# Performance work log

Measured on AMD Instinct MI355X. Metric: run time of the kernel, lower is better.

The kernel has to match this reference:

```python
import jax, jax.numpy as jnp
import numpy as np

N = 50000
E = 800000
NODE_IN = 128
HID = 256
OUT = 256
EDGE_DIM = 16
HEADS = 4
CH = HID // HEADS  # 64
NEG_SLOPE = 0.2


def _init_linear(key, fan_in, fan_out):
    k1, k2 = jax.random.split(key)
    bound = 1.0 / np.sqrt(fan_in)
    W = jax.random.uniform(k1, (fan_in, fan_out), jnp.float32, -bound, bound)
    b = jax.random.uniform(k2, (fan_out,), jnp.float32, -bound, bound)
    return W, b


def setup_inputs() -> dict:
    key = jax.random.key(0)
    ks = jax.random.split(key, 12)
    node_feats = jax.random.normal(ks[0], (N, NODE_IN), jnp.float32)
    edge_index = jax.random.randint(ks[1], (2, E), 0, N, jnp.int64)
    edge_attr = jax.random.normal(ks[2], (E, EDGE_DIM), jnp.float32)

    Wnp, bnp = _init_linear(ks[3], NODE_IN, HID)           # node_proj
    Wep, bep = _init_linear(ks[4], EDGE_DIM, HID)          # edge_proj
    # GATConv 1: in = 2*HID, out per head = CH
    Wg1, _ = _init_linear(ks[5], 2 * HID, HEADS * CH)
    as1 = jax.random.normal(ks[6], (HEADS, CH), jnp.float32) * 0.1
    ad1 = jax.random.normal(ks[7], (HEADS, CH), jnp.float32) * 0.1
    bg1 = jnp.zeros((HEADS * CH,), jnp.float32)
    # GATConv 2: in = HID, out per head = OUT//HEADS
    Wg2, _ = _init_linear(ks[8], HID, HEADS * (OUT // HEADS))
    as2 = jax.random.normal(ks[9], (HEADS, OUT // HEADS), jnp.float32) * 0.1
    ad2 = jax.random.normal(ks[10], (HEADS, OUT // HEADS), jnp.float32) * 0.1
    bg2 = jnp.zeros((OUT,), jnp.float32)
    Wo, bo = _init_linear(ks[11], OUT, OUT)                # out_proj
    return {
        "node_feats": node_feats, "edge_attr": edge_attr,
        "Wnp": Wnp, "bnp": bnp, "Wep": Wep, "bep": bep,
        "Wg1": Wg1, "as1": as1, "ad1": ad1, "bg1": bg1,
        "Wg2": Wg2, "as2": as2, "ad2": ad2, "bg2": bg2,
        "Wo": Wo, "bo": bo,
        "edge_index": edge_index,
    }


def scatter_mean(src, index, num_nodes):
    # mean of edge features grouped by target node; empty groups -> 0 (count clamped to 1)
    s = jax.ops.segment_sum(src, index, num_segments=num_nodes)
    cnt = jax.ops.segment_sum(jnp.ones((src.shape[0],), src.dtype), index, num_segments=num_nodes)
    return s / jnp.maximum(cnt, 1.0)[:, None]


def gat_conv(x, src, dst, W, att_src, att_dst, bias, num_nodes, heads, ch):
    # PyG GATConv with add_self_loops=True (loops appended by caller via src/dst),
    # concat=True, negative_slope=0.2.
    xh = (x @ W).reshape(num_nodes, heads, ch)             # [N,H,C]
    a_src = jnp.sum(xh * att_src, axis=-1)                 # [N,H]
    a_dst = jnp.sum(xh * att_dst, axis=-1)                 # [N,H]
    logits = jax.nn.leaky_relu(a_src[src] + a_dst[dst], NEG_SLOPE)  # [E,H]
    # segment softmax over incoming edges of each destination node
    m = jax.ops.segment_max(logits, dst, num_segments=num_nodes)    # [N,H]
    ex = jnp.exp(logits - m[dst])
    denom = jax.ops.segment_sum(ex, dst, num_segments=num_nodes)    # [N,H]
    alpha = ex / denom[dst]                                          # [E,H]
    msg = xh[src] * alpha[:, :, None]                                # [E,H,C]
    out = jax.ops.segment_sum(msg, dst, num_segments=num_nodes)      # [N,H,C]
    return out.reshape(num_nodes, heads * ch) + bias


def reference(node_feats, edge_attr, Wnp, bnp, Wep, bep,
              Wg1, as1, ad1, bg1, Wg2, as2, ad2, bg2, Wo, bo, edge_index):
    n = node_feats.shape[0]
    x = node_feats @ Wnp + bnp                                       # [N,HID]
    # EdgeAggregator: mean of edge_attr over target nodes, then edge_proj
    nef = scatter_mean(edge_attr, edge_index[1], n)                  # [N,EDGE_DIM]
    nef = nef @ Wep + bep                                            # [N,HID]
    x = jnp.concatenate([x, nef], axis=-1)                           # [N,2*HID]
    # add self loops once (same augmented edge set for both GAT layers)
    loops = jnp.arange(n, dtype=edge_index.dtype)
    src = jnp.concatenate([edge_index[0], loops])
    dst = jnp.concatenate([edge_index[1], loops])
    x = jax.nn.elu(gat_conv(x, src, dst, Wg1, as1, ad1, bg1, n, HEADS, CH))
    # dropout is identity in eval mode
    x = jax.nn.elu(gat_conv(x, src, dst, Wg2, as2, ad2, bg2, n, HEADS, OUT // HEADS))
    return x @ Wo + bo
```

## Files before the change

### kernel.cpp

```cpp
#include <hip/hip_runtime.h>
#include <hip/hip_bf16.h>


#define HEADS 4

typedef __attribute__((ext_vector_type(8))) _Float16 f16x8;
typedef __attribute__((ext_vector_type(4))) float f32x4;
typedef __attribute__((ext_vector_type(4))) unsigned short u16x4;
typedef __attribute__((ext_vector_type(8))) unsigned short u16x8;

__device__ __forceinline__ unsigned short f2h(float v) {
    _Float16 h = (_Float16)v;
    return __builtin_bit_cast(unsigned short, h);
}
__device__ __forceinline__ float h2f(unsigned short u) {
    return (float)__builtin_bit_cast(_Float16, u);
}
__device__ __forceinline__ void split_hilo16(float v, unsigned short& h, unsigned short& l) {
    h = f2h(v);
    l = f2h(v - h2f(h));
}
__device__ __forceinline__ void gl2lds16(const unsigned short* g, unsigned short* l) {
    __builtin_amdgcn_global_load_lds(
        (const __attribute__((address_space(1))) unsigned int*)g,
        (__attribute__((address_space(3))) unsigned int*)l,
        16, 0, 0);
}


__global__ __launch_bounds__(256) void count_kernel(
    const int* __restrict__ dst, int* __restrict__ cnt, int E)
{
    int e = blockIdx.x * 256 + threadIdx.x;
    if (e < E) atomicAdd(&cnt[dst[e]], 1);
}

__global__ __launch_bounds__(256) void scan1_kernel(
    const int* __restrict__ cnt, int* __restrict__ chunk_sum, int N)
{
    __shared__ int sd[256];
    int t = threadIdx.x;
    int n = blockIdx.x * 256 + t;
    sd[t] = (n < N) ? (cnt[n] + 1) : 0;
    __syncthreads();
    for (int o = 128; o > 0; o >>= 1) {
        if (t < o) sd[t] += sd[t + o];
        __syncthreads();
    }
    if (t == 0) chunk_sum[blockIdx.x] = sd[0];
}

__global__ __launch_bounds__(256) void scan2_kernel(
    const int* __restrict__ chunk_sum, int* __restrict__ chunk_off, int nchunk)
{
    __shared__ int sd[256];
    __shared__ int carry;
    int t = threadIdx.x;
    if (t == 0) carry = 0;
    __syncthreads();
    for (int b = 0; b < nchunk; b += 256) {
        int i = b + t;
        int v = (i < nchunk) ? chunk_sum[i] : 0;
        sd[t] = v;
        __syncthreads();
        for (int o = 1; o < 256; o <<= 1) {
            int x = (t >= o) ? sd[t - o] : 0;
            __syncthreads();
            sd[t] += x;
            __syncthreads();
        }
        if (i < nchunk) chunk_off[i] = carry + sd[t] - v;
        __syncthreads();
        if (t == 0) carry += sd[255];
        __syncthreads();
    }
}

__global__ __launch_bounds__(256) void scan3_kernel(
    const int* __restrict__ cnt, const int* __restrict__ chunk_off,
    int* __restrict__ rowptr, int* __restrict__ fillptr,
    int* __restrict__ col, int* __restrict__ eid, int N)
{
    __shared__ int sd[256];
    int t = threadIdx.x;
    int n = blockIdx.x * 256 + t;
    int v = (n < N) ? (cnt[n] + 1) : 0;
    sd[t] = v;
    __syncthreads();
    for (int o = 1; o < 256; o <<= 1) {
        int x = (t >= o) ? sd[t - o] : 0;
        __syncthreads();
        sd[t] += x;
        __syncthreads();
    }
    if (n < N) {
        int incl = sd[t];
        int r = chunk_off[blockIdx.x] + incl - v;
        rowptr[n] = r;
        col[r] = n;
        eid[r] = -1;
        fillptr[n] = r + 1;
        if (n == N - 1) rowptr[N] = chunk_off[blockIdx.x] + incl;
    }
}

__global__ __launch_bounds__(256) void fill_kernel(
    const int* __restrict__ src, const int* __restrict__ dst,
    int* __restrict__ fillptr, int* __restrict__ col, int* __restrict__ eid, int E)
{
    int e = blockIdx.x * 256 + threadIdx.x;
    if (e >= E) return;
    int d = dst[e];
    int p = atomicAdd(&fillptr[d], 1);
    col[p] = src[e];
    eid[p] = e;
}

__global__ __launch_bounds__(256) void nef_csr_kernel(
    const float* __restrict__ ea, const int* __restrict__ rowptr,
    const int* __restrict__ eid,
    unsigned short* __restrict__ nefF, int N)
{
    int n = blockIdx.x * 4 + (threadIdx.x >> 6);
    if (n >= N) return;
    int t = threadIdx.x & 63;
    int f = t & 15, g = t >> 4;
    int base = rowptr[n], end = rowptr[n + 1];
    int deg = end - base - 1;
    float acc = 0.0f;
    for (int j = base + 1 + g; j < end; j += 4) {
        int e = eid[j];
        acc += ea[(size_t)e * 16 + f];
    }
    acc += __shfl_down(acc, 32, 64);
    acc += __shfl_down(acc, 16, 64);
    if (t < 16) {
        float v = acc / fmaxf((float)deg, 1.0f);
        nefF[(size_t)n * 32 + t] = f2h(v);
    } else if (t < 32) {
        nefF[(size_t)n * 32 + t] = 0;
    }
}

__global__ __launch_bounds__(256) void compose_w1_kernel(
    const float* __restrict__ Wnp, const float* __restrict__ Wep,
    const float* __restrict__ bnp, const float* __restrict__ bep,
    const float* __restrict__ Wg1,
    float* __restrict__ Wc, float* __restrict__ c1)
{
    int idx = blockIdx.x * 256 + threadIdx.x;
    if (idx >= 145 * 256) return;
    int i = idx >> 8, j = idx & 255;
    float s = 0.0f;
    if (i < 128) {
        for (int k = 0; k < 256; k++) s += Wnp[i * 256 + k] * Wg1[(size_t)k * 256 + j];
        Wc[i * 256 + j] = s;
    } else if (i < 144) {
        int ii = i - 128;
        for (int k = 0; k < 256; k++) s += Wep[ii * 256 + k] * Wg1[(size_t)(256 + k) * 256 + j];
        Wc[i * 256 + j] = s;
    } else {
        for (int k = 0; k < 256; k++)
            s += bnp[k] * Wg1[(size_t)k * 256 + j] + bep[k] * Wg1[(size_t)(256 + k) * 256 + j];
        c1[j] = s;
    }
}

__device__ __forceinline__ void pack_one(
    const float* __restrict__ W, int K, int KP, int idx,
    unsigned short* __restrict__ Ph, unsigned short* __restrict__ Pl)
{
    int tile = idx >> 9, w = idx & 511, lane = w >> 3, j = w & 7;
    int nk = KP >> 5;
    int ctile = tile / nk, t = tile % nk;
    int k = t * 32 + ((lane >> 4) << 3) + j;
    int n = (ctile << 4) + (lane & 15);
    float v = (k < K) ? W[(size_t)k * 256 + n] : 0.0f;
    unsigned short h, l;
    split_hilo16(v, h, l);
    Ph[idx] = h;
    Pl[idx] = l;
}

__global__ __launch_bounds__(256) void pack3_w_kernel(
    const float* __restrict__ Wc,  unsigned short* __restrict__ PcH,  unsigned short* __restrict__ PcL,
    const float* __restrict__ Wg2, unsigned short* __restrict__ Pg2H, unsigned short* __restrict__ Pg2L,
    const float* __restrict__ Wo,  unsigned short* __restrict__ PoH,  unsigned short* __restrict__ PoL)
{
    const int S0 = 160 * 256;
    const int S1 = S0 + 256 * 256;
    const int S2 = S1 + 256 * 256;
    int idx = blockIdx.x * 256 + threadIdx.x;
    if (idx < S0) {
        pack_one(Wc, 144, 160, idx, PcH, PcL);
    } else if (idx < S1) {
        pack_one(Wg2, 256, 256, idx - S0, Pg2H, Pg2L);
    } else if (idx < S2) {
        pack_one(Wo, 256, 256, idx - S1, PoH, PoL);
    }
}

template <int KSTEPS, int AMODE, int OMODE, bool FUSE_ATT>
__global__ __launch_bounds__(256, 4) void mfma_gemm_kernel(
    const unsigned short* __restrict__ Ah, const unsigned short* __restrict__ Al,
    const float* __restrict__ Af32,
    int lda,
    const unsigned short* __restrict__ Ph, const unsigned short* __restrict__ Pl,
    const float* __restrict__ bias,
    float* __restrict__ Cf,
    unsigned short* __restrict__ Ch, unsigned short* __restrict__ Cl,
    int ldc, int col_off, int Nrows,
    const float* __restrict__ att_src, const float* __restrict__ att_dst,
    float* __restrict__ a_srcO, float* __restrict__ a_dstO)
{
    __shared__ unsigned short ldsB[2][2][8][512];
    int tid = threadIdx.x;
    int wave = tid >> 6, lane = tid & 63;
    int quad = lane >> 4, m16 = lane & 15;
    int rowblk = blockIdx.x, colhalf = blockIdx.y;
    int ctile0 = colhalf * 8;

    int row = rowblk * 64 + wave * 16 + m16;
    bool rowok = row < Nrows;

    auto stage = [&](int t, int buf) {
        #pragma unroll
        for (int q = 0; q < 2; q++) {
            int c = wave * 2 + q;
            size_t gb = ((size_t)((ctile0 + c) * KSTEPS + t)) * 512 + lane * 8;
            gl2lds16(Ph + gb, &ldsB[buf][0][c][0]);
            gl2lds16(Pl + gb, &ldsB[buf][1][c][0]);
        }
    };

    u16x8 aH[KSTEPS];
    u16x8 aL[AMODE == 0 ? KSTEPS : 1];
    f32x4 aF[AMODE == 3 ? 2 * KSTEPS : 1];
    #pragma unroll
    for (int t = 0; t < KSTEPS; t++) {
        if (AMODE == 3) {
            if (t < KSTEPS - 1) {
                aF[2 * t] = (f32x4){};
                aF[2 * t + 1] = (f32x4){};
                if (rowok) {
                    const float* p = Af32 + (size_t)row * 128 + t * 32 + quad * 8;
                    aF[2 * t]     = *(const f32x4*)p;
                    aF[2 * t + 1] = *(const f32x4*)(p + 4);
                }
            } else {
                aH[t] = (u16x8){};
                if (rowok) aH[t] = *(const u16x8*)(Ah + (size_t)row * 32 + quad * 8);
            }
        } else {
            int k = t * 32 + quad * 8;
            aH[t] = (u16x8){};
            if (rowok) aH[t] = *(const u16x8*)(Ah + (size_t)row * lda + k);
            if (AMODE == 0) {
                aL[t] = (u16x8){};
                if (rowok) aL[t] = *(const u16x8*)(Al + (size_t)row * lda + k);
            }
        }
    }

    f32x4 acc[8] = {};
    stage(0, 0);
    __syncthreads();

    #pragma unroll
    for (int t = 0; t < KSTEPS; t++) {
        const int buf = t & 1;
        if (t + 1 < KSTEPS) stage(t + 1, buf ^ 1);

        f16x8 a_h, a_l;
        if (AMODE == 3 && t < KSTEPS - 1) {
            #pragma unroll
            for (int i = 0; i < 4; i++) {
                ((_Float16*)&a_h)[i]     = (_Float16)aF[2 * t][i];
                ((_Float16*)&a_h)[4 + i] = (_Float16)aF[2 * t + 1][i];
            }
        } else {
            a_h = __builtin_bit_cast(f16x8, aH[t]);
        }
        if (AMODE == 0) a_l = __builtin_bit_cast(f16x8, aL[t]);

        #pragma unroll
        for (int c = 0; c < 8; c++) {
            f16x8 b_h = __builtin_bit_cast(f16x8, *(const u16x8*)&ldsB[buf][0][c][lane * 8]);
            f16x8 b_l = __builtin_bit_cast(f16x8, *(const u16x8*)&ldsB[buf][1][c][lane * 8]);
            acc[c] = __builtin_amdgcn_mfma_f32_16x16x32_f16(a_h, b_h, acc[c], 0, 0, 0);
            if (AMODE == 0)
                acc[c] = __builtin_amdgcn_mfma_f32_16x16x32_f16(a_l, b_h, acc[c], 0, 0, 0);
            acc[c] = __builtin_amdgcn_mfma_f32_16x16x32_f16(a_h, b_l, acc[c], 0, 0, 0);
        }
        if (t + 1 < KSTEPS) __syncthreads();
    }

    #pragma unroll
    for (int c = 0; c < 8; c++) {
        int ocol = (ctile0 + c) * 16 + m16;
        float bv = bias ? bias[ocol] : 0.0f;
        #pragma unroll
        for (int r = 0; r < 4; r++) {
            int orow = rowblk * 64 + wave * 16 + quad * 4 + r;
            if (orow >= Nrows) continue;
            float v = acc[c][r] + bv;
            size_t oidx = (size_t)orow * ldc + col_off + ocol;
            if (OMODE == 1) {
                unsigned short h, l;
                split_hilo16(v, h, l);
                Ch[oidx] = h;
                Cl[oidx] = l;
            } else if (OMODE == 2) {
                Ch[oidx] = f2h(v);
            } else {
                Cf[oidx] = v;
            }
        }
    }

    if (FUSE_ATT) {
        float ps[4][2] = {}, pd[4][2] = {};
        #pragma unroll
        for (int c = 0; c < 8; c++) {
            int ocol = (ctile0 + c) * 16 + m16;
            float bv = bias ? bias[ocol] : 0.0f;
            float asv = att_src[ocol];
            float adv = att_dst[ocol];
            int hl = c >> 2;
            #pragma unroll
            for (int r = 0; r < 4; r++) {
                float v = acc[c][r] + bv;
                ps[r][hl] += v * asv;
                pd[r][hl] += v * adv;
            }
        }
        #pragma unroll
        for (int r = 0; r < 4; r++) {
            #pragma unroll
            for (int hl = 0; hl < 2; hl++) {
                float s = ps[r][hl], d = pd[r][hl];
                #pragma unroll
                for (int o = 8; o > 0; o >>= 1) {
                    s += __shfl_down(s, o, 64);
                    d += __shfl_down(d, o, 64);
                }
                if (m16 == 0) {
                    int orow = rowblk * 64 + wave * 16 + quad * 4 + r;
                    if (orow < Nrows) {
                        int gh = colhalf * 2 + hl;
                        a_srcO[orow * 4 + gh] = s;
                        a_dstO[orow * 4 + gh] = d;
                    }
                }
            }
        }
    }
}

template <bool OUTF16>
__global__ __launch_bounds__(256) void gat_agg_csr_kernel(
    const unsigned short* __restrict__ xh,
    const int* __restrict__ rowptr, const int* __restrict__ col,
    const float* __restrict__ a_src, const float* __restrict__ a_dst,
    const float* __restrict__ bias,
    unsigned short* __restrict__ outA, unsigned short* __restrict__ outB, int N)
{
    __shared__ float wlds[4][128][HEADS];
    int t = threadIdx.x;
    int wv = t >> 6;
    int n = blockIdx.x * 4 + wv;
    if (n >= N) return;
    int c = t & 63;
    int h = c >> 4;
    int base = rowptr[n], end = rowptr[n + 1];
    int deg = end - base;
    int e1 = end - 1;
    float4 ad = *(const float4*)&a_dst[n * 4];
    float adh = (h == 0) ? ad.x : (h == 1) ? ad.y : (h == 2) ? ad.z : ad.w;
    const unsigned short* xcol = xh + (c << 2);

    float4 acc = {0.0f, 0.0f, 0.0f, 0.0f};
    float den = 0.0f;

    if (deg <= 128) {
        float4 ds = {0.0f, 0.0f, 0.0f, 0.0f};
        for (int j = base + c; j < end; j += 64) {
            int s = col[j];
            float4 as4 = *(const float4*)&a_src[s * 4];
            float l0 = as4.x + ad.x, l1 = as4.y + ad.y;
            float l2 = as4.z + ad.z, l3 = as4.w + ad.w;
            l0 = fmaxf(l0, 0.2f * l0);
            l1 = fmaxf(l1, 0.2f * l1);
            l2 = fmaxf(l2, 0.2f * l2);
            l3 = fmaxf(l3, 0.2f * l3);
            float4 wv4 = {__expf(l0), __expf(l1), __expf(l2), __expf(l3)};
            *(float4*)&wlds[wv][j - base][0] = wv4;
            ds.x += wv4.x; ds.y += wv4.y; ds.z += wv4.z; ds.w += wv4.w;
        }
        #pragma unroll
        for (int o = 32; o > 0; o >>= 1) {
            ds.x += __shfl_down(ds.x, o, 64);
            ds.y += __shfl_down(ds.y, o, 64);
            ds.z += __shfl_down(ds.z, o, 64);
            ds.w += __shfl_down(ds.w, o, 64);
        }
        float d0 = __shfl(ds.x, 0, 64);
        float d1 = __shfl(ds.y, 0, 64);
        float d2 = __shfl(ds.z, 0, 64);
        float d3 = __shfl(ds.w, 0, 64);
        den = (h == 0) ? d0 : (h == 1) ? d1 : (h == 2) ? d2 : d3;

        for (int j = base; j < end; j += 4) {
            int j1 = j + 1 < e1 ? j + 1 : e1;
            int j2 = j + 2 < e1 ? j + 2 : e1;
            int j3 = j + 3 < e1 ? j + 3 : e1;
            int s0 = col[j], s1 = col[j1], s2 = col[j2], s3 = col[j3];
            float w0 = wlds[wv][j - base][h];
            float w1 = (j + 1 < end) ? wlds[wv][j1 - base][h] : 0.0f;
            float w2 = (j + 2 < end) ? wlds[wv][j2 - base][h] : 0.0f;
            float w3 = (j + 3 < end) ? wlds[wv][j3 - base][h] : 0.0f;
            u16x4 x0 = *(const u16x4*)(xcol + (size_t)s0 * 256);
            u16x4 x1 = *(const u16x4*)(xcol + (size_t)s1 * 256);
            u16x4 x2 = *(const u16x4*)(xcol + (size_t)s2 * 256);
            u16x4 x3 = *(const u16x4*)(xcol + (size_t)s3 * 256);
            acc.x += w0 * h2f(x0[0]) + w1 * h2f(x1[0]) + w2 * h2f(x2[0]) + w3 * h2f(x3[0]);
            acc.y += w0 * h2f(x0[1]) + w1 * h2f(x1[1]) + w2 * h2f(x2[1]) + w3 * h2f(x3[1]);
            acc.z += w0 * h2f(x0[2]) + w1 * h2f(x1[2]) + w2 * h2f(x2[2]) + w3 * h2f(x3[2]);
            acc.w += w0 * h2f(x0[3]) + w1 * h2f(x1[3]) + w2 * h2f(x2[3]) + w3 * h2f(x3[3]);
        }
    } else {
        for (int j = base; j < end; j += 4) {
            int j1 = j + 1 < e1 ? j + 1 : e1;
            int j2 = j + 2 < e1 ? j + 2 : e1;
            int j3 = j + 3 < e1 ? j + 3 : e1;
            int s0 = col[j], s1 = col[j1], s2 = col[j2], s3 = col[j3];
            float l0 = a_src[s0 * 4 + h] + adh;
            float l1 = a_src[s1 * 4 + h] + adh;
            float l2 = a_src[s2 * 4 + h] + adh;
            float l3 = a_src[s3 * 4 + h] + adh;
            l0 = fmaxf(l0, 0.2f * l0);
            l1 = fmaxf(l1, 0.2f * l1);
            l2 = fmaxf(l2, 0.2f * l2);
            l3 = fmaxf(l3, 0.2f * l3);
            float w0 = __expf(l0);
            float w1 = (j + 1 < end) ? __expf(l1) : 0.0f;
            float w2 = (j + 2 < end) ? __expf(l2) : 0.0f;
            float w3 = (j + 3 < end) ? __expf(l3) : 0.0f;
            u16x4 x0 = *(const u16x4*)(xcol + (size_t)s0 * 256);
            u16x4 x1 = *(const u16x4*)(xcol + (size_t)s1 * 256);
            u16x4 x2 = *(const u16x4*)(xcol + (size_t)s2 * 256);
            u16x4 x3 = *(const u16x4*)(xcol + (size_t)s3 * 256);
            den += (w0 + w1) + (w2 + w3);
            acc.x += w0 * h2f(x0[0]) + w1 * h2f(x1[0]) + w2 * h2f(x2[0]) + w3 * h2f(x3[0]);
            acc.y += w0 * h2f(x0[1]) + w1 * h2f(x1[1]) + w2 * h2f(x2[1]) + w3 * h2f(x3[1]);
            acc.z += w0 * h2f(x0[2]) + w1 * h2f(x1[2]) + w2 * h2f(x2[2]) + w3 * h2f(x3[2]);
            acc.w += w0 * h2f(x0[3]) + w1 * h2f(x1[3]) + w2 * h2f(x2[3]) + w3 * h2f(x3[3]);
        }
    }

    float inv = 1.0f / den;
    float4 bv = *(const float4*)(bias + (c << 2));
    float o0 = acc.x * inv + bv.x;
    float o1 = acc.y * inv + bv.y;
    float o2 = acc.z * inv + bv.z;
    float o3 = acc.w * inv + bv.w;
    o0 = (o0 > 0.0f) ? o0 : (__expf(o0) - 1.0f);
    o1 = (o1 > 0.0f) ? o1 : (__expf(o1) - 1.0f);
    o2 = (o2 > 0.0f) ? o2 : (__expf(o2) - 1.0f);
    o3 = (o3 > 0.0f) ? o3 : (__expf(o3) - 1.0f);
    if (OUTF16) {
        u16x4 H;
        H[0] = f2h(o0); H[1] = f2h(o1); H[2] = f2h(o2); H[3] = f2h(o3);
        *(u16x4*)(&outA[(size_t)n * 256 + (c << 2)]) = H;
    } else {
        u16x4 H, L;
        split_hilo16(o0, ((unsigned short*)&H)[0], ((unsigned short*)&L)[0]);
        split_hilo16(o1, ((unsigned short*)&H)[1], ((unsigned short*)&L)[1]);
        split_hilo16(o2, ((unsigned short*)&H)[2], ((unsigned short*)&L)[2]);
        split_hilo16(o3, ((unsigned short*)&H)[3], ((unsigned short*)&L)[3]);
        *(u16x4*)(&outA[(size_t)n * 256 + (c << 2)]) = H;
        *(u16x4*)(&outB[(size_t)n * 256 + (c << 2)]) = L;
    }
}


extern "C" void kernel_launch(void* const* d_in, const int* in_sizes, int n_in,
                              void* d_out, int out_size, void* d_ws, size_t ws_size,
                              hipStream_t stream)
{
    const float* node_feats = (const float*)d_in[0];
    const float* edge_attr  = (const float*)d_in[1];
    const float* Wnp = (const float*)d_in[2];
    const float* bnp = (const float*)d_in[3];
    const float* Wep = (const float*)d_in[4];
    const float* bep = (const float*)d_in[5];
    const float* Wg1 = (const float*)d_in[6];
    const float* as1 = (const float*)d_in[7];
    const float* ad1 = (const float*)d_in[8];
    const float* bg1 = (const float*)d_in[9];
    const float* Wg2 = (const float*)d_in[10];
    const float* as2 = (const float*)d_in[11];
    const float* ad2 = (const float*)d_in[12];
    const float* bg2 = (const float*)d_in[13];
    const float* Wo  = (const float*)d_in[14];
    const float* bo  = (const float*)d_in[15];
    const int*   ei  = (const int*)d_in[16];

    const int N = in_sizes[0] / 128;
    const int E = in_sizes[16] / 2;
    const int* src = ei;
    const int* dst = ei + E;
    const int nchunk = (N + 255) / 256;
    const int EN = E + N;

    typedef unsigned short u16;

    char* base = (char*)d_ws;
    size_t off = 0;
    auto alloc = [&](size_t bytes) -> char* {
        char* p = base + off;
        off += (bytes + 255) & ~(size_t)255;
        return p;
    };
    u16* xhh  = (u16*)alloc((size_t)N * 256 * 2);
    u16* x3F  = (u16*)alloc((size_t)N * 256 * 2);
    u16* R3   = (u16*)alloc((size_t)N * 512 * 2);
    u16* nefF = (u16*)alloc((size_t)N * 32 * 2);
    float* a_src = (float*)alloc((size_t)N * 4 * 4);
    float* a_dst = (float*)alloc((size_t)N * 4 * 4);
    float* Wc    = (float*)alloc(144 * 256 * 4);
    float* c1    = (float*)alloc(256 * 4);
    u16* PcH  = (u16*)alloc(160 * 256 * 2);
    u16* PcL  = (u16*)alloc(160 * 256 * 2);
    u16* Pg2H = (u16*)alloc(256 * 256 * 2);
    u16* Pg2L = (u16*)alloc(256 * 256 * 2);
    u16* PoH  = (u16*)alloc(256 * 256 * 2);
    u16* PoL  = (u16*)alloc(256 * 256 * 2);
    int* cnt       = (int*)alloc((size_t)N * 4);
    int* rowptr    = (int*)alloc((size_t)(N + 1) * 4);
    int* fillptr   = (int*)alloc((size_t)N * 4);
    int* chunk_sum = (int*)alloc((size_t)nchunk * 4);
    int* chunk_off = (int*)alloc((size_t)nchunk * 4);
    int* colv      = (int*)alloc((size_t)EN * 4);
    int* eid       = (int*)alloc((size_t)EN * 4);

    u16* x4H = R3;
    u16* x4L = R3 + (size_t)N * 256;

    float* out = (float*)d_out;
    dim3 ggrid((N + 63) / 64, 2);

    hipMemsetAsync(cnt, 0, (size_t)N * sizeof(int), stream);
    count_kernel<<<(E + 255) / 256, 256, 0, stream>>>(dst, cnt, E);
    scan1_kernel<<<nchunk, 256, 0, stream>>>(cnt, chunk_sum, N);
    scan2_kernel<<<1, 256, 0, stream>>>(chunk_sum, chunk_off, nchunk);
    scan3_kernel<<<nchunk, 256, 0, stream>>>(cnt, chunk_off, rowptr, fillptr, colv, eid, N);
    fill_kernel<<<(E + 255) / 256, 256, 0, stream>>>(src, dst, fillptr, colv, eid, E);

    nef_csr_kernel<<<(N + 3) / 4, 256, 0, stream>>>(edge_attr, rowptr, eid, nefF, N);
    compose_w1_kernel<<<145, 256, 0, stream>>>(Wnp, Wep, bnp, bep, Wg1, Wc, c1);
    {
        const int total = 160 * 256 + 256 * 256 + 256 * 256;
        pack3_w_kernel<<<(total + 255) / 256, 256, 0, stream>>>(
            Wc, PcH, PcL, Wg2, Pg2H, Pg2L, Wo, PoH, PoL);
    }

    mfma_gemm_kernel<5, 3, 2, true><<<ggrid, 256, 0, stream>>>(
        nefF, nullptr, node_feats, 160, PcH, PcL, c1, nullptr, xhh, nullptr,
        256, 0, N, as1, ad1, a_src, a_dst);
    gat_agg_csr_kernel<true><<<(N + 3) / 4, 256, 0, stream>>>(
        xhh, rowptr, colv, a_src, a_dst, bg1, x3F, nullptr, N);

    mfma_gemm_kernel<8, 1, 2, true><<<ggrid, 256, 0, stream>>>(
        x3F, nullptr, nullptr, 256, Pg2H, Pg2L, nullptr, nullptr, xhh, nullptr,
        256, 0, N, as2, ad2, a_src, a_dst);
    gat_agg_csr_kernel<false><<<(N + 3) / 4, 256, 0, stream>>>(
        xhh, rowptr, colv, a_src, a_dst, bg2, x4H, x4L, N);

    mfma_gemm_kernel<8, 0, 0, false><<<ggrid, 256, 0, stream>>>(
        x4H, x4L, nullptr, 256, PoH, PoL, bo, out, nullptr, nullptr,
        256, 0, N, nullptr, nullptr, nullptr, nullptr);
}
```

Measured before the change: 533.1 us.

## Retile MFMA GEMM to 128-row by 64-column blocks with full-K B preload

The GEMM kernel is retiled so each block covers 128 rows and 4 column tiles (one head), with each wave computing two 16-row fragments. All K steps of B are loaded into LDS once up front, replacing the double-buffered per-step staging and its per-step barriers. A fragments are loaded inside the K loop instead of being preloaded into registers, and the attention-logit fusion now maps one head per block column. LDS use grows with KSTEPS and launch bounds drop to 2 blocks per SM, which can reduce occupancy.

```diff
diff --git a/kernel.cpp b/kernel.cpp
--- a/kernel.cpp
+++ b/kernel.cpp
@@ -201,7 +201,7 @@
 }
 
 template <int KSTEPS, int AMODE, int OMODE, bool FUSE_ATT>
-__global__ __launch_bounds__(256, 4) void mfma_gemm_kernel(
+__global__ __launch_bounds__(256, 2) void mfma_gemm_kernel(
     const unsigned short* __restrict__ Ah, const unsigned short* __restrict__ Al,
     const float* __restrict__ Af32,
     int lda,
@@ -213,143 +213,138 @@
     const float* __restrict__ att_src, const float* __restrict__ att_dst,
     float* __restrict__ a_srcO, float* __restrict__ a_dstO)
 {
-    __shared__ unsigned short ldsB[2][2][8][512];
+    __shared__ unsigned short ldsB[2][4][KSTEPS * 512];
     int tid = threadIdx.x;
     int wave = tid >> 6, lane = tid & 63;
     int quad = lane >> 4, m16 = lane & 15;
-    int rowblk = blockIdx.x, colhalf = blockIdx.y;
-    int ctile0 = colhalf * 8;
-
-    int row = rowblk * 64 + wave * 16 + m16;
-    bool rowok = row < Nrows;
-
-    auto stage = [&](int t, int buf) {
+    int rowblk = blockIdx.x, cq = blockIdx.y;
+    int ctile0 = cq * 4;
+
+    int row0 = rowblk * 128 + wave * 32 + m16;
+    int row1 = row0 + 16;
+    bool ok0 = row0 < Nrows, ok1 = row1 < Nrows;
+
+    {
+        int c = wave;
         #pragma unroll
-        for (int q = 0; q < 2; q++) {
-            int c = wave * 2 + q;
+        for (int t = 0; t < KSTEPS; t++) {
             size_t gb = ((size_t)((ctile0 + c) * KSTEPS + t)) * 512 + lane * 8;
-            gl2lds16(Ph + gb, &ldsB[buf][0][c][0]);
-            gl2lds16(Pl + gb, &ldsB[buf][1][c][0]);
-        }
-    };
-
-    u16x8 aH[KSTEPS];
-    u16x8 aL[AMODE == 0 ? KSTEPS : 1];
-    f32x4 aF[AMODE == 3 ? 2 * KSTEPS : 1];
+            gl2lds16(Ph + gb, &ldsB[0][c][t * 512]);
+            gl2lds16(Pl + gb, &ldsB[1][c][t * 512]);
+        }
+    }
+
+    f32x4 acc[2][4] = {};
+    __syncthreads();
+
     #pragma unroll
     for (int t = 0; t < KSTEPS; t++) {
+        f16x8 a0 = {}, a1 = {}, al0 = {}, al1 = {};
         if (AMODE == 3) {
             if (t < KSTEPS - 1) {
-                aF[2 * t] = (f32x4){};
-                aF[2 * t + 1] = (f32x4){};
-                if (rowok) {
-                    const float* p = Af32 + (size_t)row * 128 + t * 32 + quad * 8;
-                    aF[2 * t]     = *(const f32x4*)p;
-                    aF[2 * t + 1] = *(const f32x4*)(p + 4);
+                if (ok0) {
+                    const float* p = Af32 + (size_t)row0 * 128 + t * 32 + quad * 8;
+                    f32x4 x = *(const f32x4*)p, y = *(const f32x4*)(p + 4);
+                    #pragma unroll
+                    for (int i = 0; i < 4; i++) {
+                        ((_Float16*)&a0)[i] = (_Float16)x[i];
+                        ((_Float16*)&a0)[4 + i] = (_Float16)y[i];
+                    }
+                }
+                if (ok1) {
+                    const float* p = Af32 + (size_t)row1 * 128 + t * 32 + quad * 8;
+                    f32x4 x = *(const f32x4*)p, y = *(const f32x4*)(p + 4);
+                    #pragma unroll
+                    for (int i = 0; i < 4; i++) {
+                        ((_Float16*)&a1)[i] = (_Float16)x[i];
+                        ((_Float16*)&a1)[4 + i] = (_Float16)y[i];
+                    }
                 }
             } else {
-                aH[t] = (u16x8){};
-                if (rowok) aH[t] = *(const u16x8*)(Ah + (size_t)row * 32 + quad * 8);
+                if (ok0) a0 = __builtin_bit_cast(f16x8, *(const u16x8*)(Ah + (size_t)row0 * 32 + quad * 8));
+                if (ok1) a1 = __builtin_bit_cast(f16x8, *(const u16x8*)(Ah + (size_t)row1 * 32 + quad * 8));
             }
         } else {
             int k = t * 32 + quad * 8;
-            aH[t] = (u16x8){};
-            if (rowok) aH[t] = *(const u16x8*)(Ah + (size_t)row * lda + k);
+            if (ok0) a0 = __builtin_bit_cast(f16x8, *(const u16x8*)(Ah + (size_t)row0 * lda + k));
+            if (ok1) a1 = __builtin_bit_cast(f16x8, *(const u16x8*)(Ah + (size_t)row1 * lda + k));
             if (AMODE == 0) {
-                aL[t] = (u16x8){};
-                if (rowok) aL[t] = *(const u16x8*)(Al + (size_t)row * lda + k);
+                if (ok0) al0 = __builtin_bit_cast(f16x8, *(const u16x8*)(Al + (size_t)row0 * lda + k));
+                if (ok1) al1 = __builtin_bit_cast(f16x8, *(const u16x8*)(Al + (size_t)row1 * lda + k));
             }
         }
-    }
-
-    f32x4 acc[8] = {};
-    stage(0, 0);
-    __syncthreads();
+
+        #pragma unroll
+        for (int c = 0; c < 4; c++) {
+            f16x8 b_h = __builtin_bit_cast(f16x8, *(const u16x8*)&ldsB[0][c][t * 512 + lane * 8]);
+            f16x8 b_l = __builtin_bit_cast(f16x8, *(const u16x8*)&ldsB[1][c][t * 512 + lane * 8]);
+            acc[0][c] = __builtin_amdgcn_mfma_f32_16x16x32_f16(a0, b_h, acc[0][c], 0, 0, 0);
+            if (AMODE == 0)
+                acc[0][c] = __builtin_amdgcn_mfma_f32_16x16x32_f16(al0, b_h, acc[0][c], 0, 0, 0);
+            acc[0][c] = __builtin_amdgcn_mfma_f32_16x16x32_f16(a0, b_l, acc[0][c], 0, 0, 0);
+            acc[1][c] = __builtin_amdgcn_mfma_f32_16x16x32_f16(a1, b_h, acc[1][c], 0, 0, 0);
+            if (AMODE == 0)
+                acc[1][c] = __builtin_amdgcn_mfma_f32_16x16x32_f16(al1, b_h, acc[1][c], 0, 0, 0);
+            acc[1][c] = __builtin_amdgcn_mfma_f32_16x16x32_f16(a1, b_l, acc[1][c], 0, 0, 0);
+        }
+    }
 
     #pragma unroll
-    for (int t = 0; t < KSTEPS; t++) {
-        const int buf = t & 1;
-        if (t + 1 < KSTEPS) stage(t + 1, buf ^ 1);
-
-        f16x8 a_h, a_l;
-        if (AMODE == 3 && t < KSTEPS - 1) {
-            #pragma unroll
-            for (int i = 0; i < 4; i++) {
-                ((_Float16*)&a_h)[i]     = (_Float16)aF[2 * t][i];
-                ((_Float16*)&a_h)[4 + i] = (_Float16)aF[2 * t + 1][i];
-            }
-        } else {
-            a_h = __builtin_bit_cast(f16x8, aH[t]);
-        }
-        if (AMODE == 0) a_l = __builtin_bit_cast(f16x8, aL[t]);
-
+    for (int f = 0; f < 2; f++) {
         #pragma unroll
-        for (int c = 0; c < 8; c++) {
-            f16x8 b_h = __builtin_bit_cast(f16x8, *(const u16x8*)&ldsB[buf][0][c][lane * 8]);
-            f16x8 b_l = __builtin_bit_cast(f16x8, *(const u16x8*)&ldsB[buf][1][c][lane * 8]);
-            acc[c] = __builtin_amdgcn_mfma_f32_16x16x32_f16(a_h, b_h, acc[c], 0, 0, 0);
-            if (AMODE == 0)
-                acc[c] = __builtin_amdgcn_mfma_f32_16x16x32_f16(a_l, b_h, acc[c], 0, 0, 0);
-            acc[c] = __builtin_amdgcn_mfma_f32_16x16x32_f16(a_h, b_l, acc[c], 0, 0, 0);
-        }
-        if (t + 1 < KSTEPS) __syncthreads();
-    }
-
-    #pragma unroll
-    for (int c = 0; c < 8; c++) {
-        int ocol = (ctile0 + c) * 16 + m16;
-        float bv = bias ? bias[ocol] : 0.0f;
-        #pragma unroll
-        for (int r = 0; r < 4; r++) {
-            int orow = rowblk * 64 + wave * 16 + quad * 4 + r;
-            if (orow >= Nrows) continue;
-            float v = acc[c][r] + bv;
-            size_t oidx = (size_t)orow * ldc + col_off + ocol;
-            if (OMODE == 1) {
-                unsigned short h, l;
-                split_hilo16(v, h, l);
-                Ch[oidx] = h;
-                Cl[oidx] = l;
-            } else if (OMODE == 2) {
-                Ch[oidx] = f2h(v);
-            } else {
-                Cf[oidx] = v;
-            }
-        }
-    }
-
-    if (FUSE_ATT) {
-        float ps[4][2] = {}, pd[4][2] = {};
-        #pragma unroll
-        for (int c = 0; c < 8; c++) {
+        for (int c = 0; c < 4; c++) {
             int ocol = (ctile0 + c) * 16 + m16;
             float bv = bias ? bias[ocol] : 0.0f;
-            float asv = att_src[ocol];
-            float adv = att_dst[ocol];
-            int hl = c >> 2;
             #pragma unroll
             for (int r = 0; r < 4; r++) {
-                float v = acc[c][r] + bv;
-                ps[r][hl] += v * asv;
-                pd[r][hl] += v * adv;
+                int orow = rowblk * 128 + wave * 32 + f * 16 + quad * 4 + r;
+                if (orow >= Nrows) continue;
+                float v = acc[f][c][r] + bv;
+                size_t oidx = (size_t)orow * ldc + col_off + ocol;
+                if (OMODE == 1) {
+                    unsigned short h, l;
+                    split_hilo16(v, h, l);
+                    Ch[oidx] = h;
+                    Cl[oidx] = l;
+                } else if (OMODE == 2) {
+                    Ch[oidx] = f2h(v);
+                } else {
+                    Cf[oidx] = v;
+                }
             }
         }
+    }
+
+    if (FUSE_ATT) {
         #pragma unroll
-        for (int r = 0; r < 4; r++) {
+        for (int f = 0; f < 2; f++) {
+            float ps[4] = {}, pd[4] = {};
             #pragma unroll
-            for (int hl = 0; hl < 2; hl++) {
-                float s = ps[r][hl], d = pd[r][hl];
+            for (int c = 0; c < 4; c++) {
+                int ocol = (ctile0 + c) * 16 + m16;
+                float bv = bias ? bias[ocol] : 0.0f;
+                float asv = att_src[ocol];
+                float adv = att_dst[ocol];
+                #pragma unroll
+                for (int r = 0; r < 4; r++) {
+                    float v = acc[f][c][r] + bv;
+                    ps[r] += v * asv;
+                    pd[r] += v * adv;
+                }
+            }
+            #pragma unroll
+            for (int r = 0; r < 4; r++) {
+                float s = ps[r], d = pd[r];
                 #pragma unroll
                 for (int o = 8; o > 0; o >>= 1) {
                     s += __shfl_down(s, o, 64);
                     d += __shfl_down(d, o, 64);
                 }
                 if (m16 == 0) {
-                    int orow = rowblk * 64 + wave * 16 + quad * 4 + r;
+                    int orow = rowblk * 128 + wave * 32 + f * 16 + quad * 4 + r;
                     if (orow < Nrows) {
-                        int gh = colhalf * 2 + hl;
-                        a_srcO[orow * 4 + gh] = s;
-                        a_dstO[orow * 4 + gh] = d;
+                        a_srcO[orow * 4 + cq] = s;
+                        a_dstO[orow * 4 + cq] = d;
                     }
                 }
             }
@@ -548,7 +543,7 @@
     u16* x4L = R3 + (size_t)N * 256;
 
     float* out = (float*)d_out;
-    dim3 ggrid((N + 63) / 64, 2);
+    dim3 ggrid((N + 127) / 128, 4);
 
     hipMemsetAsync(cnt, 0, (size_t)N * sizeof(int), stream);
     count_kernel<<<(E + 255) / 256, 256, 0, stream>>>(dst, cnt, E);
```

Measured after the change: 563.0 us. 5.6% more time.
